# Performance work log

Measured on AMD Instinct MI355X. Metric: run time of the kernel, lower is better.

The kernel has to match this reference:

```python
import jax, jax.numpy as jnp
import numpy as np


def _leaky(x):
    return jnp.where(x > 0, x, 0.2 * x)


def _time_warp(x, strength, k_wp, k_sh):
    # Vectorized equivalent of the per-sample python loop in _apply_time_warp.
    B, L, Fd = x.shape
    warp_steps = (L * 0.1 * strength).astype(jnp.int32)
    wp = jax.random.randint(k_wp, (B, 1), warp_steps, L - warp_steps)
    sh = jax.random.randint(k_sh, (B, 1), -warp_steps, warp_steps + 1)
    t = jnp.arange(L)[None, :]
    # shift > 0: warped[t] = x[min(t+shift, L-1)] for t >= warp_point, else x[t]
    pos = jnp.where(t >= wp, jnp.minimum(t + sh, L - 1), t)
    # shift < 0: warped[t] = x[t - shift] for warp_point+shift <= t < L+shift, else x[t]
    neg = jnp.where((t >= wp + sh) & (t < L + sh), t - sh, t)
    idx = jnp.where(sh > 0, pos, jnp.where(sh < 0, neg, t))  # (B, L)
    warped = x[jnp.arange(B)[:, None], idx]  # gather along time -> (B, L, Fd)
    return warped


def _freq_aug(x, strength, k_f):
    fx = jnp.fft.fft(x, axis=1)
    ratio = jnp.minimum(strength * 0.1, 0.5)
    keep = jax.random.uniform(k_f, x.shape) > ratio
    res = jnp.fft.ifft(fx * keep.astype(fx.dtype), axis=1).real.astype(x.dtype)
    return jnp.where(strength < 0.01, x, res)


def _forward(x, batch_size, w1, b1, w2, b2, w3, b3, wm, bm, wn, bn, ws, bs,
             p_mask, p_noise, p_shift, p_scale):
    B, L, Fd = x.shape
    s_mask = jax.nn.sigmoid(p_mask)
    s_noise = jax.nn.sigmoid(p_noise)
    s_shift = jax.nn.sigmoid(p_shift)
    s_scale = jax.nn.sigmoid(p_scale)
    s_mix = 1.0 - s_shift

    key = jax.random.key(42)
    kz, kn, kwp, ksh, kf = jax.random.split(key, 5)

    z = jax.random.normal(kz, (B, w1.shape[0]), x.dtype)
    h = _leaky(z @ w1 + b1)
    h = _leaky(h @ w2 + b2)
    h = _leaky(h @ w3 + b3)  # (B, 2*hidden)

    mask = jax.nn.sigmoid(h @ wm + bm).reshape(B, L, Fd)
    mask = 1.0 - (1.0 - mask) * s_mask * 0.3

    noise_mag = jax.nn.softplus(h @ wn + bn).reshape(B, L, Fd)
    noise = jax.random.normal(kn, x.shape, x.dtype) * noise_mag * s_noise * 0.05

    warped = _time_warp(x, s_shift, kwp, ksh)

    scale = jax.nn.softplus(h @ ws + bs)[:, None, :]  # (B,1,Fd)
    scale = 1.0 + (scale - 0.5) * 0.2 * s_scale

    freq = _freq_aug(x, s_mix, kf)

    wa = jnp.clip(1.0 - s_mix - s_shift, 0.1, 0.8)
    wb = s_mix * 0.5
    wc = s_shift * 0.5
    tot = wa + wb + wc
    wa, wb, wc = wa / tot, wb / tot, wc / tot

    aug = x * mask * scale + noise
    aug = aug * wa + freq * wb + warped * wc
    return aug


def setup_inputs() -> dict:
    key = jax.random.key(0)
    ks = jax.random.split(key, 8)
    B, L, Fd = 256, 512, 64
    H, ND = 128, 64
    x = jax.random.normal(ks[0], (B, L, Fd), jnp.float32)

    def lin(k, i, o):
        return jax.random.normal(k, (i, o), jnp.float32) * 0.02

    inp = {
        "x": x,
        "batch_size": B,
        "w1": lin(ks[1], ND, H), "b1": jnp.zeros((H,), jnp.float32),
        "w2": lin(ks[2], H, 2 * H), "b2": jnp.zeros((2 * H,), jnp.float32),
        "w3": lin(ks[3], 2 * H, 2 * H), "b3": jnp.zeros((2 * H,), jnp.float32),
        "wm": lin(ks[4], 2 * H, L * Fd), "bm": jnp.zeros((L * Fd,), jnp.float32),
        "wn": lin(ks[5], 2 * H, L * Fd), "bn": jnp.zeros((L * Fd,), jnp.float32),
        "ws": lin(ks[6], 2 * H, Fd), "bs": jnp.zeros((Fd,), jnp.float32),
        "p_mask": jnp.float32(0.5), "p_noise": jnp.float32(0.5),
        "p_shift": jnp.float32(0.5), "p_scale": jnp.float32(0.5),
    }
    return inp


def reference(x, batch_size, w1, b1, w2, b2, w3, b3, wm, bm, wn, bn, ws, bs,
              p_mask, p_noise, p_shift, p_scale):
    return _forward(x, batch_size, w1, b1, w2, b2, w3, b3, wm, bm, wn, bn,
                    ws, bs, p_mask, p_noise, p_shift, p_scale)
```

## Files before the change

kernel.cpp:

```cpp
#include <hip/hip_runtime.h>
#include <cstdint>
#include <cstddef>


typedef unsigned int u32;
typedef unsigned short u16;

#define Bd 256
#define Ld 512
#define Fd 64
#define Nd 32768

struct U2 { u32 a, b; };

__device__ __forceinline__ u32 rotl32(u32 x, int r){ return (x << r) | (x >> (32 - r)); }

__device__ __forceinline__ U2 tf2x32(u32 k0, u32 k1, u32 x0, u32 x1){
  u32 ks2 = k0 ^ k1 ^ 0x1BD11BDAu;
  x0 += k0; x1 += k1;
#define TFR4(r0,r1,r2,r3) \
  x0 += x1; x1 = rotl32(x1, r0); x1 ^= x0; \
  x0 += x1; x1 = rotl32(x1, r1); x1 ^= x0; \
  x0 += x1; x1 = rotl32(x1, r2); x1 ^= x0; \
  x0 += x1; x1 = rotl32(x1, r3); x1 ^= x0;
  TFR4(13,15,26,6)  x0 += k1;  x1 += ks2 + 1u;
  TFR4(17,29,16,24) x0 += ks2; x1 += k0 + 2u;
  TFR4(13,15,26,6)  x0 += k0;  x1 += k1 + 3u;
  TFR4(17,29,16,24) x0 += k1;  x1 += ks2 + 4u;
  TFR4(13,15,26,6)  x0 += ks2; x1 += k0 + 5u;
#undef TFR4
  U2 r; r.a = x0; r.b = x1; return r;
}

__device__ __forceinline__ u32 rb32(u32 k0, u32 k1, u32 i){
  U2 r = tf2x32(k0, k1, 0u, i);
  return r.a ^ r.b;
}

__device__ __forceinline__ U2 split_key(u32 k0, u32 k1, u32 j){
  return tf2x32(k0, k1, 0u, j);
}

__device__ __forceinline__ float sigmoidf_(float x){ return 1.0f / (1.0f + expf(-x)); }
__device__ __forceinline__ float softplusf_(float x){ return fmaxf(x, 0.0f) + log1pf(expf(-fabsf(x))); }
__device__ __forceinline__ float leakyf_(float x){ return (x > 0.0f) ? x : 0.2f * x; }

__device__ __forceinline__ float erfinvf_(float x){
  float w = -log1pf(-x * x);
  float p;
  if (w < 5.0f){
    w -= 2.5f;
    p =               2.81022636e-08f;
    p = fmaf(p, w,    3.43273939e-07f);
    p = fmaf(p, w,   -3.5233877e-06f);
    p = fmaf(p, w,   -4.39150654e-06f);
    p = fmaf(p, w,    0.00021858087f);
    p = fmaf(p, w,   -0.00125372503f);
    p = fmaf(p, w,   -0.00417768164f);
    p = fmaf(p, w,    0.246640727f);
    p = fmaf(p, w,    1.50140941f);
  } else {
    w = sqrtf(w) - 3.0f;
    p =              -0.000200214257f;
    p = fmaf(p, w,    0.000100950558f);
    p = fmaf(p, w,    0.00134934322f);
    p = fmaf(p, w,   -0.00367342844f);
    p = fmaf(p, w,    0.00573950773f);
    p = fmaf(p, w,   -0.0076224613f);
    p = fmaf(p, w,    0.00943887047f);
    p = fmaf(p, w,    1.00167406f);
    p = fmaf(p, w,    2.83297682f);
  }
  return p * x;
}

__device__ __forceinline__ float uniform_from_bits(u32 bits){
  return __uint_as_float((bits >> 9) | 0x3f800000u) - 1.0f;
}

__device__ __forceinline__ float normal_from_bits(u32 bits){
  float u01 = uniform_from_bits(bits);
  const float lo = -0.99999994f;
  float v = fmaf(u01, 2.0f, lo);
  v = fmaxf(lo, v);
  return 1.41421356f * erfinvf_(v);
}

__device__ __forceinline__ int warp_idx_(int t, int wp, int sh){
  int tps = t + sh;
  int pos = (t >= wp) ? ((tps < Ld - 1) ? tps : (Ld - 1)) : t;
  int neg = ((t >= wp + sh) && (t < Ld + sh)) ? (t - sh) : t;
  return (sh > 0) ? pos : ((sh < 0) ? neg : t);
}

__device__ __forceinline__ u32 pack_bf16_2(float a, float b){
  u32 ua = __float_as_uint(a), ub = __float_as_uint(b);
  u32 ra = (ua + 0x7FFFu + ((ua >> 16) & 1u)) >> 16;
  u32 rb = (ub + 0x7FFFu + ((ub >> 16) & 1u)) >> 16;
  return (ra & 0xFFFFu) | (rb << 16);
}
__device__ __forceinline__ u16 f2bf(float a){
  u32 ua = __float_as_uint(a);
  return (u16)((ua + 0x7FFFu + ((ua >> 16) & 1u)) >> 16);
}
__device__ __forceinline__ float bf2f(u16 v){
  return __uint_as_float(((u32)v) << 16);
}

__device__ __forceinline__ int swz_(int v){
  return ((v >> 2) & 7) ^ ((v & 3) << 1);
}
__device__ __forceinline__ int rev9_(int k){
  return (int)(__brev((u32)k) >> 23);
}

__global__ __launch_bounds__(256) void k_init(float* __restrict__ z, int* __restrict__ wp,
                                              int* __restrict__ shv, const float* __restrict__ p_shift){
  int gid = blockIdx.x * 256 + threadIdx.x;
  U2 kz = split_key(0u, 42u, 0u);
  z[gid] = normal_from_bits(rb32(kz.a, kz.b, (u32)gid));
  if (blockIdx.x == 0){
    int b = threadIdx.x;
    float s_shift = sigmoidf_(p_shift[0]);
    int wsteps = (int)(51.2f * s_shift);
    U2 kwp = split_key(0u, 42u, 2u);
    U2 ksh = split_key(0u, 42u, 3u);
    {
      U2 k1 = split_key(kwp.a, kwp.b, 0u);
      U2 k2 = split_key(kwp.a, kwp.b, 1u);
      u32 hi = rb32(k1.a, k1.b, (u32)b);
      u32 lo = rb32(k2.a, k2.b, (u32)b);
      u32 span = (u32)(Ld - 2 * wsteps);
      u32 mult = 65536u % span; mult = (mult * mult) % span;
      u32 off = ((hi % span) * mult + (lo % span)) % span;
      wp[b] = wsteps + (int)off;
    }
    {
      U2 k1 = split_key(ksh.a, ksh.b, 0u);
      U2 k2 = split_key(ksh.a, ksh.b, 1u);
      u32 hi = rb32(k1.a, k1.b, (u32)b);
      u32 lo = rb32(k2.a, k2.b, (u32)b);
      u32 span = (u32)(2 * wsteps + 1);
      u32 mult = 65536u % span; mult = (mult * mult) % span;
      u32 off = ((hi % span) * mult + (lo % span)) % span;
      shv[b] = -wsteps + (int)off;
    }
  }
}

__global__ __launch_bounds__(128) void k_mlp1(const float* __restrict__ z, const float* __restrict__ w1,
                                              const float* __restrict__ b1, float* __restrict__ h1){
  int b = blockIdx.x, n = threadIdx.x;
  const float* zr = z + b * 64;
  float acc = b1[n];
  #pragma unroll 8
  for (int k = 0; k < 64; ++k) acc = fmaf(zr[k], w1[k * 128 + n], acc);
  h1[b * 128 + n] = leakyf_(acc);
}

__global__ __launch_bounds__(256) void k_mlp2(const float* __restrict__ h1, const float* __restrict__ w2,
                                              const float* __restrict__ b2, float* __restrict__ h2){
  int b = blockIdx.x, n = threadIdx.x;
  const float* hr = h1 + b * 128;
  float acc = b2[n];
  #pragma unroll 8
  for (int k = 0; k < 128; ++k) acc = fmaf(hr[k], w2[k * 256 + n], acc);
  h2[b * 256 + n] = leakyf_(acc);
}

__global__ __launch_bounds__(256) void k_mlp3(const float* __restrict__ h2, const float* __restrict__ w3,
                                              const float* __restrict__ b3, u16* __restrict__ h3b){
  int b = blockIdx.x, n = threadIdx.x;
  const float* hr = h2 + b * 256;
  float acc = b3[n];
  #pragma unroll 8
  for (int k = 0; k < 256; ++k) acc = fmaf(hr[k], w3[k * 256 + n], acc);
  h3b[b * 256 + n] = f2bf(leakyf_(acc));
}

__global__ __launch_bounds__(256) void k_scale(const u16* __restrict__ h3b, const float* __restrict__ wsc,
                                               const float* __restrict__ bsc, const float* __restrict__ p_scale,
                                               float* __restrict__ scl){
  int tid = threadIdx.x;
  int b = blockIdx.x * 4 + (tid >> 6);
  int f = tid & 63;
  float acc = bsc[f];
  for (int k = 0; k < 256; ++k) acc = fmaf(bf2f(h3b[b * 256 + k]), wsc[k * 64 + f], acc);
  float s_scale = sigmoidf_(p_scale[0]);
  scl[b * 64 + f] = 1.0f + (softplusf_(acc) - 0.5f) * 0.2f * s_scale;
}

typedef short short8 __attribute__((ext_vector_type(8)));
typedef float f32x4 __attribute__((ext_vector_type(4)));
union Frag { uint4 u; short8 s; };

__global__ __launch_bounds__(256, 2) void k_gemm(
    const u16* __restrict__ h3b,
    const float* __restrict__ wm, const float* __restrict__ bm,
    const float* __restrict__ wn, const float* __restrict__ bn,
    u16* __restrict__ logM, u16* __restrict__ logN)
{
  __shared__ __align__(16) u32 As [128 * 32];
  __shared__ __align__(16) u32 Bs0[128 * 32];
  __shared__ __align__(16) u32 Bs1[128 * 32];

  const int tid  = threadIdx.x;
  const int lane = tid & 63;
  const int w    = tid >> 6;
  const int q    = lane >> 4;
  const int lo   = lane & 15;
  const int nt0  = blockIdx.x << 7;
  const int b0   = blockIdx.y << 7;
  const int wr   = (w >> 1) << 6;
  const int wc   = (w & 1) << 6;

  const int p  = lane >> 3;
  const int c8 = lane & 7;
  const int nb = (w << 5) + (p << 2);

  f32x4 accm[4][4], accn[4][4];
  #pragma unroll
  for (int i = 0; i < 4; ++i)
    #pragma unroll
    for (int j = 0; j < 4; ++j){ accm[i][j] = (f32x4)0.0f; accn[i][j] = (f32x4)0.0f; }

  for (int kc = 0; kc < 256; kc += 64){
    if (kc) __syncthreads();
    #pragma unroll
    for (int j = 0; j < 4; ++j){
      int idx  = j * 256 + tid;
      int row  = idx >> 3;
      int slot = idx & 7;
      int g    = slot ^ swz_(row);
      uint4 v  = *(const uint4*)(h3b + (size_t)(b0 + row) * 256 + kc + g * 8);
      *(uint4*)&As[row * 32 + slot * 4] = v;
    }
    #pragma unroll
    for (int cp = 0; cp < 4; ++cp){
      int c = cp * 8 + c8;
      size_t gb = (size_t)(kc + 2 * c) * Nd + nt0 + nb;
      float4 m0 = *(const float4*)(wm + gb);
      float4 m1 = *(const float4*)(wm + gb + Nd);
      float4 v0 = *(const float4*)(wn + gb);
      float4 v1 = *(const float4*)(wn + gb + Nd);
      int g = c >> 2, cl = c & 3;
      #pragma unroll
      for (int s = 0; s < 4; ++s){
        int n = nb + s;
        int addr = n * 32 + (g ^ swz_(n)) * 4 + cl;
        float a0 = (s == 0) ? m0.x : (s == 1) ? m0.y : (s == 2) ? m0.z : m0.w;
        float a1 = (s == 0) ? m1.x : (s == 1) ? m1.y : (s == 2) ? m1.z : m1.w;
        float b0f = (s == 0) ? v0.x : (s == 1) ? v0.y : (s == 2) ? v0.z : v0.w;
        float b1f = (s == 0) ? v1.x : (s == 1) ? v1.y : (s == 2) ? v1.z : v1.w;
        Bs0[addr] = pack_bf16_2(a0, a1);
        Bs1[addr] = pack_bf16_2(b0f, b1f);
      }
    }
    __syncthreads();

    #pragma unroll
    for (int u = 0; u < 2; ++u){
      int G = u * 4 + q;
      Frag af[4], bfm[4], bfn[4];
      #pragma unroll
      for (int mt = 0; mt < 4; ++mt){
        int row = wr + mt * 16 + lo;
        af[mt].u = *(const uint4*)&As[row * 32 + (G ^ swz_(row)) * 4];
      }
      #pragma unroll
      for (int nt = 0; nt < 4; ++nt){
        int n = wc + nt * 16 + lo;
        int ad = n * 32 + (G ^ swz_(n)) * 4;
        bfm[nt].u = *(const uint4*)&Bs0[ad];
        bfn[nt].u = *(const uint4*)&Bs1[ad];
      }
      #pragma unroll
      for (int mt = 0; mt < 4; ++mt){
        #pragma unroll
        for (int nt = 0; nt < 4; ++nt){
          accm[mt][nt] = __builtin_amdgcn_mfma_f32_16x16x32_bf16(af[mt].s, bfm[nt].s, accm[mt][nt], 0, 0, 0);
          accn[mt][nt] = __builtin_amdgcn_mfma_f32_16x16x32_bf16(af[mt].s, bfn[nt].s, accn[mt][nt], 0, 0, 0);
        }
      }
    }
  }

  #pragma unroll
  for (int nt = 0; nt < 4; ++nt){
    int n = nt0 + wc + nt * 16 + lo;
    float bmv = bm[n];
    float bnv = bn[n];
    #pragma unroll
    for (int mt = 0; mt < 4; ++mt){
      #pragma unroll
      for (int r = 0; r < 4; ++r){
        int b = b0 + wr + mt * 16 + q * 4 + r;
        size_t o = (size_t)b * Nd + n;
        logM[o] = f2bf(accm[mt][nt][r] + bmv);
        logN[o] = f2bf(accn[mt][nt][r] + bnv);
      }
    }
  }
}

#define PITCH 529

__device__ __forceinline__ int lphys(int t){ return t + (t >> 5); }

__global__ __launch_bounds__(256, 4) void k_faug(
    const float* __restrict__ x,
    const u16* __restrict__ logM, const u16* __restrict__ logN,
    const float* __restrict__ scl,
    const int* __restrict__ wp, const int* __restrict__ shv,
    const float* __restrict__ p_mask, const float* __restrict__ p_noise,
    const float* __restrict__ p_shift,
    float* __restrict__ out)
{
  __shared__ float SR[8 * PITCH];
  __shared__ float SI[8 * PITCH];
  __shared__ float2 tw[256];

  const int tid = threadIdx.x;
  const int b   = blockIdx.x >> 2;
  const int f0  = (blockIdx.x & 3) << 4;

  float s_mask  = sigmoidf_(p_mask[0]);
  float s_noise = sigmoidf_(p_noise[0]);
  float s_shift = sigmoidf_(p_shift[0]);
  float s_mix   = 1.0f - s_shift;
  float ratio   = fminf(s_mix * 0.1f, 0.5f);
  float wa = 1.0f - s_mix - s_shift;
  wa = fminf(fmaxf(wa, 0.1f), 0.8f);
  float wb = s_mix * 0.5f;
  float wc = s_shift * 0.5f;
  float tot = wa + wb + wc;
  wa /= tot; wb /= tot; wc /= tot;
  bool pass = (s_mix < 0.01f);

  U2 kf  = split_key(0u, 42u, 4u);
  U2 knk = split_key(0u, 42u, 1u);
  const int wpb = wp[b];
  const int shb = shv[b];

  {
    float ang = -6.283185307179586f * ((float)tid / 512.0f);
    tw[tid] = make_float2(cosf(ang), sinf(ang));
  }

  const float* xb = x + (size_t)b * Nd;
  #pragma unroll
  for (int s = 0; s < 8; ++s){
    int qq = (s << 8) + tid;
    int t  = qq >> 2;
    int f4 = qq & 3;
    float4 v = *(const float4*)(xb + t * 64 + f0 + (f4 << 2));
    int j = f4 << 1;
    int pt = lphys(t);
    SR[j * PITCH + pt]       = v.x;  SI[j * PITCH + pt]       = v.y;
    SR[(j + 1) * PITCH + pt] = v.z;  SI[(j + 1) * PITCH + pt] = v.w;
  }
  __syncthreads();

  for (int s = 9; s >= 1; --s){
    int half = 1 << (s - 1);
    #pragma unroll
    for (int it = 0; it < 8; ++it){
      int j  = it;
      int bi = tid;
      int pos = bi & (half - 1);
      int g = bi >> (s - 1);
      int i1 = (g << s) + pos;
      int i2 = i1 + half;
      int a1 = j * PITCH + lphys(i1);
      int a2 = j * PITCH + lphys(i2);
      float ur = SR[a1], ui = SI[a1];
      float vr = SR[a2], vi = SI[a2];
      SR[a1] = ur + vr; SI[a1] = ui + vi;
      float dr = ur - vr, di = ui - vi;
      float2 w = tw[pos << (9 - s)];
      SR[a2] = dr * w.x - di * w.y;
      SI[a2] = dr * w.y + di * w.x;
    }
    __syncthreads();
  }

  #pragma unroll
  for (int it = 0; it < 8; ++it){
    int j = it;
    int k = tid;
    int nItr = (k == 0) ? 2 : 1;
    for (int e = 0; e < nItr; ++e){
      int kk = (e == 0) ? k : 256;
      int nk = (512 - kk) & 511;
      int pk = rev9_(kk), pn = rev9_(nk);
      int ak = j * PITCH + lphys(pk);
      int an = j * PITCH + lphys(pn);
      float zkr = SR[ak], zki = SI[ak];
      float znr = SR[an], zni = SI[an];
      float X0r = 0.5f * (zkr + znr), X0i = 0.5f * (zki - zni);
      float X1r = 0.5f * (zki + zni), X1i = 0.5f * (znr - zkr);
      int fA = f0 + (j << 1);
      u32 ck = (u32)((b * Ld + kk) * Fd + fA);
      u32 cn = (u32)((b * Ld + nk) * Fd + fA);
      float k0a = (uniform_from_bits(rb32(kf.a, kf.b, ck))      > ratio) ? 1.0f : 0.0f;
      float k0b = (uniform_from_bits(rb32(kf.a, kf.b, cn))      > ratio) ? 1.0f : 0.0f;
      float k1a = (uniform_from_bits(rb32(kf.a, kf.b, ck + 1u)) > ratio) ? 1.0f : 0.0f;
      float k1b = (uniform_from_bits(rb32(kf.a, kf.b, cn + 1u)) > ratio) ? 1.0f : 0.0f;
      float m0 = 0.5f * (k0a + k0b);
      float m1 = 0.5f * (k1a + k1b);
      SR[ak] = m0 * X0r - m1 * X1i;
      SI[ak] = m0 * X0i + m1 * X1r;
      SR[an] = m0 * X0r + m1 * X1i;
      SI[an] = m1 * X1r - m0 * X0i;
    }
  }
  __syncthreads();

  for (int s = 1; s <= 9; ++s){
    int half = 1 << (s - 1);
    #pragma unroll
    for (int it = 0; it < 8; ++it){
      int j  = it;
      int bi = tid;
      int pos = bi & (half - 1);
      int g = bi >> (s - 1);
      int i1 = (g << s) + pos;
      int i2 = i1 + half;
      int a1 = j * PITCH + lphys(i1);
      int a2 = j * PITCH + lphys(i2);
      float2 w = tw[pos << (9 - s)];
      float vr = SR[a2], vi = SI[a2];
      float tx_ = vr * w.x + vi * w.y;
      float ty_ = vi * w.x - vr * w.y;
      float ur = SR[a1], ui = SI[a1];
      SR[a1] = ur + tx_; SI[a1] = ui + ty_;
      SR[a2] = ur - tx_; SI[a2] = ui - ty_;
    }
    __syncthreads();
  }

  const float inv512 = 1.0f / 512.0f;
  const u16* lMb = logM + (size_t)b * Nd;
  const u16* lNb = logN + (size_t)b * Nd;
  float* ob = out + (size_t)b * Nd;
  #pragma unroll
  for (int s = 0; s < 8; ++s){
    int qq = (s << 8) + tid;
    int t  = qq >> 2;
    int f4 = qq & 3;
    int f  = f0 + (f4 << 2);
    int j  = f4 << 1;
    int pt = lphys(t);
    int nidx = t * 64 + f;
    float4 xv = *(const float4*)(xb + nidx);
    int wi = warp_idx_(t, wpb, shb);
    float4 wv = *(const float4*)(xb + wi * 64 + f);
    float4 sc = *(const float4*)(scl + b * 64 + f);
    ushort4 mr = *(const ushort4*)(lMb + nidx);
    ushort4 nr4 = *(const ushort4*)(lNb + nidx);
    float fr[4];
    fr[0] = SR[j * PITCH + pt] * inv512;
    fr[1] = SI[j * PITCH + pt] * inv512;
    fr[2] = SR[(j + 1) * PITCH + pt] * inv512;
    fr[3] = SI[(j + 1) * PITCH + pt] * inv512;
    const float xvv[4] = {xv.x, xv.y, xv.z, xv.w};
    const float wvv[4] = {wv.x, wv.y, wv.z, wv.w};
    const float scv[4] = {sc.x, sc.y, sc.z, sc.w};
    const u16 mrv[4] = {mr.x, mr.y, mr.z, mr.w};
    const u16 nrv[4] = {nr4.x, nr4.y, nr4.z, nr4.w};
    float o[4];
    #pragma unroll
    for (int c = 0; c < 4; ++c){
      float maskv = sigmoidf_(bf2f(mrv[c]));
      maskv = 1.0f - (1.0f - maskv) * s_mask * 0.3f;
      float nmag = softplusf_(bf2f(nrv[c]));
      float nz = normal_from_bits(rb32(knk.a, knk.b, (u32)(b * Nd + nidx + c)));
      float noise = nz * nmag * s_noise * 0.05f;
      float fq = pass ? xvv[c] : fr[c];
      float aug = fmaf(xvv[c] * maskv, scv[c], noise);
      o[c] = aug * wa + fq * wb + wvv[c] * wc;
    }
    *(float4*)(ob + nidx) = make_float4(o[0], o[1], o[2], o[3]);
  }
}

extern "C" void kernel_launch(void* const* d_in, const int* in_sizes, int n_in,
                              void* d_out, int out_size, void* d_ws, size_t ws_size,
                              hipStream_t stream)
{
  (void)in_sizes; (void)n_in; (void)out_size; (void)ws_size;
  const float* x   = (const float*)d_in[0];
  const float* w1  = (const float*)d_in[2];
  const float* b1  = (const float*)d_in[3];
  const float* w2  = (const float*)d_in[4];
  const float* b2  = (const float*)d_in[5];
  const float* w3  = (const float*)d_in[6];
  const float* b3  = (const float*)d_in[7];
  const float* wm  = (const float*)d_in[8];
  const float* bm  = (const float*)d_in[9];
  const float* wn  = (const float*)d_in[10];
  const float* bn  = (const float*)d_in[11];
  const float* wsc = (const float*)d_in[12];
  const float* bsc = (const float*)d_in[13];
  const float* pm  = (const float*)d_in[14];
  const float* pn  = (const float*)d_in[15];
  const float* psh = (const float*)d_in[16];
  const float* psc = (const float*)d_in[17];
  float* out = (float*)d_out;
  char* ws = (char*)d_ws;

  int*   wp   = (int*)(ws + 0);
  int*   shv  = (int*)(ws + 1024);
  float* z    = (float*)(ws + 2048);
  float* h1   = (float*)(ws + 67584);
  float* h2   = (float*)(ws + 198656);
  u16*   h3b  = (u16*)  (ws + 460800);
  float* scl  = (float*)(ws + 591872);
  u16*   logM = (u16*)  (ws + 1048576);
  u16*   logN = (u16*)  (ws + 1048576 + 16777216);

  k_init <<<dim3(64),      dim3(256), 0, stream>>>(z, wp, shv, psh);
  k_mlp1 <<<dim3(256),     dim3(128), 0, stream>>>(z, w1, b1, h1);
  k_mlp2 <<<dim3(256),     dim3(256), 0, stream>>>(h1, w2, b2, h2);
  k_mlp3 <<<dim3(256),     dim3(256), 0, stream>>>(h2, w3, b3, h3b);
  k_scale<<<dim3(64),      dim3(256), 0, stream>>>(h3b, wsc, bsc, psc, scl);
  k_gemm <<<dim3(256, 2),  dim3(256), 0, stream>>>(h3b, wm, bm, wn, bn, logM, logN);
  k_faug <<<dim3(1024),    dim3(256), 0, stream>>>(x, logM, logN, scl, wp, shv,
                                                   pm, pn, psh, out);
}
```

Measured before the change: 326.2 us.

## Use radix-4 FFT passes with interleaved complex LDS and fuse z generation into MLP1

The forward and inverse 512-point FFTs in the fused augmentation kernel now run as four radix-4 passes plus one radix-2 pass instead of nine radix-2 stages. This roughly halves the shared-memory round trips and barriers. Shared memory changes from split real/imag arrays to an interleaved float2 array with a new padding scheme, so each access is a 64-bit load. Separately, the Gaussian z vector is now generated inside k_mlp1 rather than written to and read back from global memory, and k_init shrinks to one block. The cost is more registers per thread in the FFT, which may lower occupancy, and a new bank-conflict pattern.

```diff
diff --git a/kernel.cpp b/kernel.cpp
--- a/kernel.cpp
+++ b/kernel.cpp
@@ -114,47 +114,47 @@
   return (int)(__brev((u32)k) >> 23);
 }
 
-__global__ __launch_bounds__(256) void k_init(float* __restrict__ z, int* __restrict__ wp,
-                                              int* __restrict__ shv, const float* __restrict__ p_shift){
-  int gid = blockIdx.x * 256 + threadIdx.x;
-  U2 kz = split_key(0u, 42u, 0u);
-  z[gid] = normal_from_bits(rb32(kz.a, kz.b, (u32)gid));
-  if (blockIdx.x == 0){
-    int b = threadIdx.x;
-    float s_shift = sigmoidf_(p_shift[0]);
-    int wsteps = (int)(51.2f * s_shift);
-    U2 kwp = split_key(0u, 42u, 2u);
-    U2 ksh = split_key(0u, 42u, 3u);
-    {
-      U2 k1 = split_key(kwp.a, kwp.b, 0u);
-      U2 k2 = split_key(kwp.a, kwp.b, 1u);
-      u32 hi = rb32(k1.a, k1.b, (u32)b);
-      u32 lo = rb32(k2.a, k2.b, (u32)b);
-      u32 span = (u32)(Ld - 2 * wsteps);
-      u32 mult = 65536u % span; mult = (mult * mult) % span;
-      u32 off = ((hi % span) * mult + (lo % span)) % span;
-      wp[b] = wsteps + (int)off;
-    }
-    {
-      U2 k1 = split_key(ksh.a, ksh.b, 0u);
-      U2 k2 = split_key(ksh.a, ksh.b, 1u);
-      u32 hi = rb32(k1.a, k1.b, (u32)b);
-      u32 lo = rb32(k2.a, k2.b, (u32)b);
-      u32 span = (u32)(2 * wsteps + 1);
-      u32 mult = 65536u % span; mult = (mult * mult) % span;
-      u32 off = ((hi % span) * mult + (lo % span)) % span;
-      shv[b] = -wsteps + (int)off;
-    }
-  }
-}
-
-__global__ __launch_bounds__(128) void k_mlp1(const float* __restrict__ z, const float* __restrict__ w1,
+__global__ __launch_bounds__(256) void k_init(int* __restrict__ wp, int* __restrict__ shv,
+                                              const float* __restrict__ p_shift){
+  int b = threadIdx.x;
+  float s_shift = sigmoidf_(p_shift[0]);
+  int wsteps = (int)(51.2f * s_shift);
+  U2 kwp = split_key(0u, 42u, 2u);
+  U2 ksh = split_key(0u, 42u, 3u);
+  {
+    U2 k1 = split_key(kwp.a, kwp.b, 0u);
+    U2 k2 = split_key(kwp.a, kwp.b, 1u);
+    u32 hi = rb32(k1.a, k1.b, (u32)b);
+    u32 lo = rb32(k2.a, k2.b, (u32)b);
+    u32 span = (u32)(Ld - 2 * wsteps);
+    u32 mult = 65536u % span; mult = (mult * mult) % span;
+    u32 off = ((hi % span) * mult + (lo % span)) % span;
+    wp[b] = wsteps + (int)off;
+  }
+  {
+    U2 k1 = split_key(ksh.a, ksh.b, 0u);
+    U2 k2 = split_key(ksh.a, ksh.b, 1u);
+    u32 hi = rb32(k1.a, k1.b, (u32)b);
+    u32 lo = rb32(k2.a, k2.b, (u32)b);
+    u32 span = (u32)(2 * wsteps + 1);
+    u32 mult = 65536u % span; mult = (mult * mult) % span;
+    u32 off = ((hi % span) * mult + (lo % span)) % span;
+    shv[b] = -wsteps + (int)off;
+  }
+}
+
+__global__ __launch_bounds__(128) void k_mlp1(const float* __restrict__ w1,
                                               const float* __restrict__ b1, float* __restrict__ h1){
+  __shared__ float zs[64];
   int b = blockIdx.x, n = threadIdx.x;
-  const float* zr = z + b * 64;
+  if (n < 64){
+    U2 kz = split_key(0u, 42u, 0u);
+    zs[n] = normal_from_bits(rb32(kz.a, kz.b, (u32)(b * 64 + n)));
+  }
+  __syncthreads();
   float acc = b1[n];
   #pragma unroll 8
-  for (int k = 0; k < 64; ++k) acc = fmaf(zr[k], w1[k * 128 + n], acc);
+  for (int k = 0; k < 64; ++k) acc = fmaf(zs[k], w1[k * 128 + n], acc);
   h1[b * 128 + n] = leakyf_(acc);
 }
 
@@ -303,9 +303,9 @@
   }
 }
 
-#define PITCH 529
-
-__device__ __forceinline__ int lphys(int t){ return t + (t >> 5); }
+#define PITCH2 578
+
+__device__ __forceinline__ int fphys(int e){ return e + (e >> 3); }
 
 __global__ __launch_bounds__(256, 4) void k_faug(
     const float* __restrict__ x,
@@ -316,8 +316,7 @@
     const float* __restrict__ p_shift,
     float* __restrict__ out)
 {
-  __shared__ float SR[8 * PITCH];
-  __shared__ float SI[8 * PITCH];
+  __shared__ float2 C[8 * PITCH2];
   __shared__ float2 tw[256];
 
   const int tid = threadIdx.x;
@@ -355,34 +354,73 @@
     int f4 = qq & 3;
     float4 v = *(const float4*)(xb + t * 64 + f0 + (f4 << 2));
     int j = f4 << 1;
-    int pt = lphys(t);
-    SR[j * PITCH + pt]       = v.x;  SI[j * PITCH + pt]       = v.y;
-    SR[(j + 1) * PITCH + pt] = v.z;  SI[(j + 1) * PITCH + pt] = v.w;
+    int pt = fphys(t);
+    C[j * PITCH2 + pt]       = make_float2(v.x, v.y);
+    C[(j + 1) * PITCH2 + pt] = make_float2(v.z, v.w);
   }
   __syncthreads();
 
-  for (int s = 9; s >= 1; --s){
-    int half = 1 << (s - 1);
-    #pragma unroll
-    for (int it = 0; it < 8; ++it){
-      int j  = it;
-      int bi = tid;
-      int pos = bi & (half - 1);
-      int g = bi >> (s - 1);
-      int i1 = (g << s) + pos;
-      int i2 = i1 + half;
-      int a1 = j * PITCH + lphys(i1);
-      int a2 = j * PITCH + lphys(i2);
-      float ur = SR[a1], ui = SI[a1];
-      float vr = SR[a2], vi = SI[a2];
-      SR[a1] = ur + vr; SI[a1] = ui + vi;
-      float dr = ur - vr, di = ui - vi;
-      float2 w = tw[pos << (9 - s)];
-      SR[a2] = dr * w.x - di * w.y;
-      SI[a2] = dr * w.y + di * w.x;
+  #pragma unroll
+  for (int ps = 0; ps < 4; ++ps){
+    const int s  = 9 - 2 * ps;
+    const int q  = 1 << (s - 2);
+    const int dq = (q >= 8) ? (q + (q >> 3)) : q;
+    float2 A[4][4]; float2 TW[4][3]; int P0[4];
+    #pragma unroll
+    for (int it = 0; it < 4; ++it){
+      int G   = it * 256 + tid;
+      int j   = G >> 7;
+      int gi  = G & 127;
+      int pos = gi & (q - 1);
+      int base = ((gi >> (s - 2)) << s) + pos;
+      int t1  = pos << (9 - s);
+      TW[it][0] = tw[t1];
+      TW[it][1] = tw[t1 + 128];
+      TW[it][2] = tw[t1 << 1];
+      int p0 = j * PITCH2 + fphys(base);
+      P0[it] = p0;
+      A[it][0] = C[p0];
+      A[it][1] = C[p0 + dq];
+      A[it][2] = C[p0 + 2 * dq];
+      A[it][3] = C[p0 + 3 * dq];
+    }
+    #pragma unroll
+    for (int it = 0; it < 4; ++it){
+      float2 W1 = TW[it][0], W1b = TW[it][1], W2 = TW[it][2];
+      float2 a0 = A[it][0], a1 = A[it][1], a2 = A[it][2], a3 = A[it][3];
+      float A0r = a0.x + a2.x, A0i = a0.y + a2.y;
+      float d0r = a0.x - a2.x, d0i = a0.y - a2.y;
+      float B0r = d0r * W1.x - d0i * W1.y;
+      float B0i = d0r * W1.y + d0i * W1.x;
+      float A1r = a1.x + a3.x, A1i = a1.y + a3.y;
+      float d1r = a1.x - a3.x, d1i = a1.y - a3.y;
+      float B1r = d1r * W1b.x - d1i * W1b.y;
+      float B1i = d1r * W1b.y + d1i * W1b.x;
+      float o0r = A0r + A1r, o0i = A0i + A1i;
+      float e0r = A0r - A1r, e0i = A0i - A1i;
+      float o1r = e0r * W2.x - e0i * W2.y;
+      float o1i = e0r * W2.y + e0i * W2.x;
+      float o2r = B0r + B1r, o2i = B0i + B1i;
+      float e1r = B0r - B1r, e1i = B0i - B1i;
+      float o3r = e1r * W2.x - e1i * W2.y;
+      float o3i = e1r * W2.y + e1i * W2.x;
+      int p0 = P0[it];
+      C[p0]          = make_float2(o0r, o0i);
+      C[p0 + dq]     = make_float2(o1r, o1i);
+      C[p0 + 2 * dq] = make_float2(o2r, o2i);
+      C[p0 + 3 * dq] = make_float2(o3r, o3i);
     }
     __syncthreads();
   }
+
+  #pragma unroll
+  for (int it = 0; it < 8; ++it){
+    int p0 = it * PITCH2 + fphys(2 * tid);
+    float2 u = C[p0], v = C[p0 + 1];
+    C[p0]     = make_float2(u.x + v.x, u.y + v.y);
+    C[p0 + 1] = make_float2(u.x - v.x, u.y - v.y);
+  }
+  __syncthreads();
 
   #pragma unroll
   for (int it = 0; it < 8; ++it){
@@ -393,12 +431,12 @@
       int kk = (e == 0) ? k : 256;
       int nk = (512 - kk) & 511;
       int pk = rev9_(kk), pn = rev9_(nk);
-      int ak = j * PITCH + lphys(pk);
-      int an = j * PITCH + lphys(pn);
-      float zkr = SR[ak], zki = SI[ak];
-      float znr = SR[an], zni = SI[an];
-      float X0r = 0.5f * (zkr + znr), X0i = 0.5f * (zki - zni);
-      float X1r = 0.5f * (zki + zni), X1i = 0.5f * (znr - zkr);
+      int ak = j * PITCH2 + fphys(pk);
+      int an = j * PITCH2 + fphys(pn);
+      float2 zk = C[ak];
+      float2 zn = C[an];
+      float X0r = 0.5f * (zk.x + zn.x), X0i = 0.5f * (zk.y - zn.y);
+      float X1r = 0.5f * (zk.y + zn.y), X1i = 0.5f * (zn.x - zk.x);
       int fA = f0 + (j << 1);
       u32 ck = (u32)((b * Ld + kk) * Fd + fA);
       u32 cn = (u32)((b * Ld + nk) * Fd + fA);
@@ -408,33 +446,66 @@
       float k1b = (uniform_from_bits(rb32(kf.a, kf.b, cn + 1u)) > ratio) ? 1.0f : 0.0f;
       float m0 = 0.5f * (k0a + k0b);
       float m1 = 0.5f * (k1a + k1b);
-      SR[ak] = m0 * X0r - m1 * X1i;
-      SI[ak] = m0 * X0i + m1 * X1r;
-      SR[an] = m0 * X0r + m1 * X1i;
-      SI[an] = m1 * X1r - m0 * X0i;
+      C[ak] = make_float2(m0 * X0r - m1 * X1i, m0 * X0i + m1 * X1r);
+      C[an] = make_float2(m0 * X0r + m1 * X1i, m1 * X1r - m0 * X0i);
     }
   }
   __syncthreads();
 
-  for (int s = 1; s <= 9; ++s){
-    int half = 1 << (s - 1);
-    #pragma unroll
-    for (int it = 0; it < 8; ++it){
-      int j  = it;
-      int bi = tid;
-      int pos = bi & (half - 1);
-      int g = bi >> (s - 1);
-      int i1 = (g << s) + pos;
-      int i2 = i1 + half;
-      int a1 = j * PITCH + lphys(i1);
-      int a2 = j * PITCH + lphys(i2);
-      float2 w = tw[pos << (9 - s)];
-      float vr = SR[a2], vi = SI[a2];
-      float tx_ = vr * w.x + vi * w.y;
-      float ty_ = vi * w.x - vr * w.y;
-      float ur = SR[a1], ui = SI[a1];
-      SR[a1] = ur + tx_; SI[a1] = ui + ty_;
-      SR[a2] = ur - tx_; SI[a2] = ui - ty_;
+  #pragma unroll
+  for (int it = 0; it < 8; ++it){
+    int p0 = it * PITCH2 + fphys(2 * tid);
+    float2 u = C[p0], v = C[p0 + 1];
+    C[p0]     = make_float2(u.x + v.x, u.y + v.y);
+    C[p0 + 1] = make_float2(u.x - v.x, u.y - v.y);
+  }
+  __syncthreads();
+
+  #pragma unroll
+  for (int ps = 0; ps < 4; ++ps){
+    const int s  = 3 + 2 * ps;
+    const int q  = 1 << (s - 2);
+    const int dq = (q >= 8) ? (q + (q >> 3)) : q;
+    float2 A[4][4]; float2 TW[4][3]; int P0[4];
+    #pragma unroll
+    for (int it = 0; it < 4; ++it){
+      int G   = it * 256 + tid;
+      int j   = G >> 7;
+      int gi  = G & 127;
+      int pos = gi & (q - 1);
+      int base = ((gi >> (s - 2)) << s) + pos;
+      int t1  = pos << (9 - s);
+      TW[it][0] = tw[t1];
+      TW[it][1] = tw[t1 + 128];
+      TW[it][2] = tw[t1 << 1];
+      int p0 = j * PITCH2 + fphys(base);
+      P0[it] = p0;
+      A[it][0] = C[p0];
+      A[it][1] = C[p0 + dq];
+      A[it][2] = C[p0 + 2 * dq];
+      A[it][3] = C[p0 + 3 * dq];
+    }
+    #pragma unroll
+    for (int it = 0; it < 4; ++it){
+      float2 W1 = TW[it][0], W1b = TW[it][1], W2 = TW[it][2];
+      float2 x0 = A[it][0], x1 = A[it][1], x2 = A[it][2], x3 = A[it][3];
+      float t1x = x1.x * W2.x + x1.y * W2.y;
+      float t1y = x1.y * W2.x - x1.x * W2.y;
+      float A0r = x0.x + t1x, A0i = x0.y + t1y;
+      float A1r = x0.x - t1x, A1i = x0.y - t1y;
+      float t3x = x3.x * W2.x + x3.y * W2.y;
+      float t3y = x3.y * W2.x - x3.x * W2.y;
+      float B0r = x2.x + t3x, B0i = x2.y + t3y;
+      float B1r = x2.x - t3x, B1i = x2.y - t3y;
+      float u0x = B0r * W1.x + B0i * W1.y;
+      float u0y = B0i * W1.x - B0r * W1.y;
+      float u1x = B1r * W1b.x + B1i * W1b.y;
+      float u1y = B1i * W1b.x - B1r * W1b.y;
+      int p0 = P0[it];
+      C[p0]          = make_float2(A0r + u0x, A0i + u0y);
+      C[p0 + dq]     = make_float2(A1r + u1x, A1i + u1y);
+      C[p0 + 2 * dq] = make_float2(A0r - u0x, A0i - u0y);
+      C[p0 + 3 * dq] = make_float2(A1r - u1x, A1i - u1y);
     }
     __syncthreads();
   }
@@ -450,7 +521,7 @@
     int f4 = qq & 3;
     int f  = f0 + (f4 << 2);
     int j  = f4 << 1;
-    int pt = lphys(t);
+    int pt = fphys(t);
     int nidx = t * 64 + f;
     float4 xv = *(const float4*)(xb + nidx);
     int wi = warp_idx_(t, wpb, shb);
@@ -458,11 +529,13 @@
     float4 sc = *(const float4*)(scl + b * 64 + f);
     ushort4 mr = *(const ushort4*)(lMb + nidx);
     ushort4 nr4 = *(const ushort4*)(lNb + nidx);
+    float2 c0 = C[j * PITCH2 + pt];
+    float2 c1 = C[(j + 1) * PITCH2 + pt];
     float fr[4];
-    fr[0] = SR[j * PITCH + pt] * inv512;
-    fr[1] = SI[j * PITCH + pt] * inv512;
-    fr[2] = SR[(j + 1) * PITCH + pt] * inv512;
-    fr[3] = SI[(j + 1) * PITCH + pt] * inv512;
+    fr[0] = c0.x * inv512;
+    fr[1] = c0.y * inv512;
+    fr[2] = c1.x * inv512;
+    fr[3] = c1.y * inv512;
     const float xvv[4] = {xv.x, xv.y, xv.z, xv.w};
     const float wvv[4] = {wv.x, wv.y, wv.z, wv.w};
     const float scv[4] = {sc.x, sc.y, sc.z, sc.w};
@@ -511,7 +584,6 @@
 
   int*   wp   = (int*)(ws + 0);
   int*   shv  = (int*)(ws + 1024);
-  float* z    = (float*)(ws + 2048);
   float* h1   = (float*)(ws + 67584);
   float* h2   = (float*)(ws + 198656);
   u16*   h3b  = (u16*)  (ws + 460800);
@@ -519,8 +591,8 @@
   u16*   logM = (u16*)  (ws + 1048576);
   u16*   logN = (u16*)  (ws + 1048576 + 16777216);
 
-  k_init <<<dim3(64),      dim3(256), 0, stream>>>(z, wp, shv, psh);
-  k_mlp1 <<<dim3(256),     dim3(128), 0, stream>>>(z, w1, b1, h1);
+  k_init <<<dim3(1),       dim3(256), 0, stream>>>(wp, shv, psh);
+  k_mlp1 <<<dim3(256),     dim3(128), 0, stream>>>(w1, b1, h1);
   k_mlp2 <<<dim3(256),     dim3(256), 0, stream>>>(h1, w2, b2, h2);
   k_mlp3 <<<dim3(256),     dim3(256), 0, stream>>>(h2, w3, b3, h3b);
   k_scale<<<dim3(64),      dim3(256), 0, stream>>>(h3b, wsc, bsc, psc, scl);
```

Measured after the change: 341.6 us. 4.7% more time.

## Split noise generation into a separate pass and fuse z generation into mlp1

Applied to the files above, without the earlier changes.

Moves the Threefry normal sampling and softplus for the noise term out of the FFT augmentation kernel into a new elementwise kernel. That kernel overwrites the bf16 noise logits in place with the final scaled noise. The z sampling also moves from k_init into k_mlp1 via shared memory, so k_init shrinks to a single block. The aim is to lighten the register- and ALU-heavy k_faug, at the cost of an extra 16 MB read-modify-write pass over logN and an extra bf16 rounding of the final noise.

```diff
diff --git a/kernel.cpp b/kernel.cpp
--- a/kernel.cpp
+++ b/kernel.cpp
@@ -114,47 +114,47 @@
   return (int)(__brev((u32)k) >> 23);
 }
 
-__global__ __launch_bounds__(256) void k_init(float* __restrict__ z, int* __restrict__ wp,
-                                              int* __restrict__ shv, const float* __restrict__ p_shift){
-  int gid = blockIdx.x * 256 + threadIdx.x;
-  U2 kz = split_key(0u, 42u, 0u);
-  z[gid] = normal_from_bits(rb32(kz.a, kz.b, (u32)gid));
-  if (blockIdx.x == 0){
-    int b = threadIdx.x;
-    float s_shift = sigmoidf_(p_shift[0]);
-    int wsteps = (int)(51.2f * s_shift);
-    U2 kwp = split_key(0u, 42u, 2u);
-    U2 ksh = split_key(0u, 42u, 3u);
-    {
-      U2 k1 = split_key(kwp.a, kwp.b, 0u);
-      U2 k2 = split_key(kwp.a, kwp.b, 1u);
-      u32 hi = rb32(k1.a, k1.b, (u32)b);
-      u32 lo = rb32(k2.a, k2.b, (u32)b);
-      u32 span = (u32)(Ld - 2 * wsteps);
-      u32 mult = 65536u % span; mult = (mult * mult) % span;
-      u32 off = ((hi % span) * mult + (lo % span)) % span;
-      wp[b] = wsteps + (int)off;
-    }
-    {
-      U2 k1 = split_key(ksh.a, ksh.b, 0u);
-      U2 k2 = split_key(ksh.a, ksh.b, 1u);
-      u32 hi = rb32(k1.a, k1.b, (u32)b);
-      u32 lo = rb32(k2.a, k2.b, (u32)b);
-      u32 span = (u32)(2 * wsteps + 1);
-      u32 mult = 65536u % span; mult = (mult * mult) % span;
-      u32 off = ((hi % span) * mult + (lo % span)) % span;
-      shv[b] = -wsteps + (int)off;
-    }
-  }
-}
-
-__global__ __launch_bounds__(128) void k_mlp1(const float* __restrict__ z, const float* __restrict__ w1,
+__global__ __launch_bounds__(256) void k_init(int* __restrict__ wp, int* __restrict__ shv,
+                                              const float* __restrict__ p_shift){
+  int b = threadIdx.x;
+  float s_shift = sigmoidf_(p_shift[0]);
+  int wsteps = (int)(51.2f * s_shift);
+  U2 kwp = split_key(0u, 42u, 2u);
+  U2 ksh = split_key(0u, 42u, 3u);
+  {
+    U2 k1 = split_key(kwp.a, kwp.b, 0u);
+    U2 k2 = split_key(kwp.a, kwp.b, 1u);
+    u32 hi = rb32(k1.a, k1.b, (u32)b);
+    u32 lo = rb32(k2.a, k2.b, (u32)b);
+    u32 span = (u32)(Ld - 2 * wsteps);
+    u32 mult = 65536u % span; mult = (mult * mult) % span;
+    u32 off = ((hi % span) * mult + (lo % span)) % span;
+    wp[b] = wsteps + (int)off;
+  }
+  {
+    U2 k1 = split_key(ksh.a, ksh.b, 0u);
+    U2 k2 = split_key(ksh.a, ksh.b, 1u);
+    u32 hi = rb32(k1.a, k1.b, (u32)b);
+    u32 lo = rb32(k2.a, k2.b, (u32)b);
+    u32 span = (u32)(2 * wsteps + 1);
+    u32 mult = 65536u % span; mult = (mult * mult) % span;
+    u32 off = ((hi % span) * mult + (lo % span)) % span;
+    shv[b] = -wsteps + (int)off;
+  }
+}
+
+__global__ __launch_bounds__(128) void k_mlp1(const float* __restrict__ w1,
                                               const float* __restrict__ b1, float* __restrict__ h1){
+  __shared__ float zs[64];
   int b = blockIdx.x, n = threadIdx.x;
-  const float* zr = z + b * 64;
+  if (n < 64){
+    U2 kz = split_key(0u, 42u, 0u);
+    zs[n] = normal_from_bits(rb32(kz.a, kz.b, (u32)(b * 64 + n)));
+  }
+  __syncthreads();
   float acc = b1[n];
   #pragma unroll 8
-  for (int k = 0; k < 64; ++k) acc = fmaf(zr[k], w1[k * 128 + n], acc);
+  for (int k = 0; k < 64; ++k) acc = fmaf(zs[k], w1[k * 128 + n], acc);
   h1[b * 128 + n] = leakyf_(acc);
 }
 
@@ -303,13 +303,37 @@
   }
 }
 
+__global__ __launch_bounds__(256) void k_noise(u16* __restrict__ logN,
+                                               const float* __restrict__ p_noise){
+  int gid = blockIdx.x * 256 + threadIdx.x;
+  u32 base = (u32)gid * 8u;
+  float s_noise = sigmoidf_(p_noise[0]);
+  float sc = s_noise * 0.05f;
+  U2 knk = split_key(0u, 42u, 1u);
+
+  uint4 v = *(const uint4*)(logN + base);
+  u32 wds[4] = {v.x, v.y, v.z, v.w};
+  u32 outw[4];
+  #pragma unroll
+  for (int h = 0; h < 4; ++h){
+    u16 l0 = (u16)(wds[h] & 0xFFFFu);
+    u16 l1 = (u16)(wds[h] >> 16);
+    float nm0 = softplusf_(bf2f(l0));
+    float nm1 = softplusf_(bf2f(l1));
+    float nz0 = normal_from_bits(rb32(knk.a, knk.b, base + (u32)(2 * h)));
+    float nz1 = normal_from_bits(rb32(knk.a, knk.b, base + (u32)(2 * h + 1)));
+    outw[h] = pack_bf16_2(nz0 * nm0 * sc, nz1 * nm1 * sc);
+  }
+  *(uint4*)(logN + base) = make_uint4(outw[0], outw[1], outw[2], outw[3]);
+}
+
 #define PITCH 529
 
 __device__ __forceinline__ int lphys(int t){ return t + (t >> 5); }
 
 __global__ __launch_bounds__(256, 4) void k_faug(
     const float* __restrict__ x,
-    const u16* __restrict__ logM, const u16* __restrict__ logN,
+    const u16* __restrict__ logM, const u16* __restrict__ noiseT,
     const float* __restrict__ scl,
     const int* __restrict__ wp, const int* __restrict__ shv,
     const float* __restrict__ p_mask, const float* __restrict__ p_noise,
@@ -325,7 +349,6 @@
   const int f0  = (blockIdx.x & 3) << 4;
 
   float s_mask  = sigmoidf_(p_mask[0]);
-  float s_noise = sigmoidf_(p_noise[0]);
   float s_shift = sigmoidf_(p_shift[0]);
   float s_mix   = 1.0f - s_shift;
   float ratio   = fminf(s_mix * 0.1f, 0.5f);
@@ -336,9 +359,9 @@
   float tot = wa + wb + wc;
   wa /= tot; wb /= tot; wc /= tot;
   bool pass = (s_mix < 0.01f);
+  (void)p_noise;
 
   U2 kf  = split_key(0u, 42u, 4u);
-  U2 knk = split_key(0u, 42u, 1u);
   const int wpb = wp[b];
   const int shb = shv[b];
 
@@ -441,7 +464,7 @@
 
   const float inv512 = 1.0f / 512.0f;
   const u16* lMb = logM + (size_t)b * Nd;
-  const u16* lNb = logN + (size_t)b * Nd;
+  const u16* lNb = noiseT + (size_t)b * Nd;
   float* ob = out + (size_t)b * Nd;
   #pragma unroll
   for (int s = 0; s < 8; ++s){
@@ -473,9 +496,7 @@
     for (int c = 0; c < 4; ++c){
       float maskv = sigmoidf_(bf2f(mrv[c]));
       maskv = 1.0f - (1.0f - maskv) * s_mask * 0.3f;
-      float nmag = softplusf_(bf2f(nrv[c]));
-      float nz = normal_from_bits(rb32(knk.a, knk.b, (u32)(b * Nd + nidx + c)));
-      float noise = nz * nmag * s_noise * 0.05f;
+      float noise = bf2f(nrv[c]);
       float fq = pass ? xvv[c] : fr[c];
       float aug = fmaf(xvv[c] * maskv, scv[c], noise);
       o[c] = aug * wa + fq * wb + wvv[c] * wc;
@@ -511,7 +532,6 @@
 
   int*   wp   = (int*)(ws + 0);
   int*   shv  = (int*)(ws + 1024);
-  float* z    = (float*)(ws + 2048);
   float* h1   = (float*)(ws + 67584);
   float* h2   = (float*)(ws + 198656);
   u16*   h3b  = (u16*)  (ws + 460800);
@@ -519,12 +539,13 @@
   u16*   logM = (u16*)  (ws + 1048576);
   u16*   logN = (u16*)  (ws + 1048576 + 16777216);
 
-  k_init <<<dim3(64),      dim3(256), 0, stream>>>(z, wp, shv, psh);
-  k_mlp1 <<<dim3(256),     dim3(128), 0, stream>>>(z, w1, b1, h1);
+  k_init <<<dim3(1),       dim3(256), 0, stream>>>(wp, shv, psh);
+  k_mlp1 <<<dim3(256),     dim3(128), 0, stream>>>(w1, b1, h1);
   k_mlp2 <<<dim3(256),     dim3(256), 0, stream>>>(h1, w2, b2, h2);
   k_mlp3 <<<dim3(256),     dim3(256), 0, stream>>>(h2, w3, b3, h3b);
   k_scale<<<dim3(64),      dim3(256), 0, stream>>>(h3b, wsc, bsc, psc, scl);
   k_gemm <<<dim3(256, 2),  dim3(256), 0, stream>>>(h3b, wm, bm, wn, bn, logM, logN);
+  k_noise<<<dim3(4096),    dim3(256), 0, stream>>>(logN, pn);
   k_faug <<<dim3(1024),    dim3(256), 0, stream>>>(x, logM, logN, scl, wp, shv,
                                                    pm, pn, psh, out);
 }
```

Measured after the change: 333.4 us. +2.2%, slower.
